# Kernel optimization log

Measured on AMD Instinct MI355X. Metric: run time of the kernel, lower is better.

## Reference

```python
import jax, jax.numpy as jnp
import numpy as np

B, C, H, W = 1, 96, 128, 128
P = 4            # patch_size
E = 192          # embed_dim
DI = 384         # d_inner = expand * embed_dim
NS = 16          # d_state
R = 12           # dt_rank = ceil(E/16)
K = 4            # scan directions
NBLK = 8         # SS2D_MBs_num
GW = C // 2      # SCPA group width


def layernorm(x, g, b, eps=1e-5):
    mu = x.mean(-1, keepdims=True)
    v = x.var(-1, keepdims=True)
    return (x - mu) * jax.lax.rsqrt(v + eps) * g + b


def batchnorm(x, g, b, m, v, eps=1e-5):
    # eval-mode BatchNorm2d over channel axis 1 of (B,C,H,W)
    return (x - m[:, None, None]) * jax.lax.rsqrt(v + eps)[:, None, None] * g[:, None, None] + b[:, None, None]


def conv2d(x, w):
    return jax.lax.conv_general_dilated(x, w, (1, 1), 'SAME', dimension_numbers=('NCHW', 'OIHW', 'NCHW'))


def dwconv2d(x, w, b):
    out = jax.lax.conv_general_dilated(x, w[:, None], (1, 1), 'SAME',
                                       dimension_numbers=('NCHW', 'OIHW', 'NCHW'),
                                       feature_group_count=w.shape[0])
    return out + b[None, :, None, None]


def lrelu(x):
    return jnp.where(x >= 0, x, 0.2 * x)


def channel_attention(x, w1, w2):
    # CBAM-style: shared MLP on avg+max pooled channel descriptors, sigmoid gate
    avg = x.mean((2, 3))
    mx = x.max((2, 3))
    mlp = lambda v: jax.nn.relu(v @ w1.T) @ w2.T
    attn = jax.nn.sigmoid(mlp(avg) + mlp(mx))
    return x * attn[:, :, None, None]


def selective_scan(xs, dts, A, Bs, Cs, Dskip):
    # xs,dts: (B,K,DI,L); A: (K,DI,NS); Bs,Cs: (B,K,NS,L); Dskip: (K,DI)
    xs_t = jnp.moveaxis(xs, -1, 0)
    dts_t = jnp.moveaxis(dts, -1, 0)
    Bs_t = jnp.moveaxis(Bs, -1, 0)
    Cs_t = jnp.moveaxis(Cs, -1, 0)
    h0 = jnp.zeros(xs.shape[:3] + (NS,), xs.dtype)  # (B,K,DI,NS)

    def step(h, t):
        xt, dt, Bt, Ct = t
        h = jnp.exp(dt[..., None] * A) * h + (dt * xt)[..., None] * Bt[:, :, None, :]
        return h, jnp.sum(h * Ct[:, :, None, :], axis=-1)

    _, ys = jax.lax.scan(step, h0, (xs_t, dts_t, Bs_t, Cs_t))
    return jnp.moveaxis(ys, 0, -1) + xs * Dskip[None, :, :, None]


def ss2d_block(x, p):
    # VMamba-style VSS block: x + SS2D(LN(x)); x: (B,Hp,Wp,E)
    (ln_g, ln_b, inproj_w, conv_w, conv_b, xproj_w, dtproj_w, dtproj_b,
     Alog, Dskip, on_g, on_b, outproj_w, merge_w) = p
    Bsz, Hp, Wp, _ = x.shape
    L = Hp * Wp
    h = layernorm(x, ln_g, ln_b)
    xz = jnp.einsum('bhwd,ed->bhwe', h, inproj_w)   # (B,Hp,Wp,2*DI)
    xc, z = jnp.split(xz, 2, axis=-1)
    xc = jax.nn.silu(dwconv2d(jnp.transpose(xc, (0, 3, 1, 2)), conv_w, conv_b))  # (B,DI,Hp,Wp)
    # 4-direction cross-scan: row-major, col-major and their reverses
    xf = xc.reshape(Bsz, DI, L)
    xwh = jnp.transpose(xc, (0, 1, 3, 2)).reshape(Bsz, DI, L)
    xs = jnp.stack([xf, xwh, jnp.flip(xf, -1), jnp.flip(xwh, -1)], axis=1)  # (B,K,DI,L)
    x_dbl = jnp.einsum('bkdl,kcd->bkcl', xs, xproj_w)  # (B,K,R+2*NS,L)
    dts, Bm, Cm = jnp.split(x_dbl, [R, R + NS], axis=2)
    dts = jax.nn.softplus(jnp.einsum('bkrl,kdr->bkdl', dts, dtproj_w) + dtproj_b[None, :, :, None])
    A = -jnp.exp(Alog)
    oy = selective_scan(xs, dts, A, Bm, Cm, Dskip)  # (B,K,DI,L)
    y0 = oy[:, 0]
    y1 = jnp.transpose(oy[:, 1].reshape(Bsz, DI, Wp, Hp), (0, 1, 3, 2)).reshape(Bsz, DI, L)
    y2 = jnp.flip(oy[:, 2], -1)
    y3 = jnp.transpose(jnp.flip(oy[:, 3], -1).reshape(Bsz, DI, Wp, Hp), (0, 1, 3, 2)).reshape(Bsz, DI, L)
    y = merge_w[0] * y0 + merge_w[1] * y1 + merge_w[2] * y2 + merge_w[3] * y3  # learnable merge
    y = jnp.transpose(y, (0, 2, 1)).reshape(Bsz, Hp, Wp, DI)
    y = layernorm(y, on_g, on_b) * jax.nn.silu(z)
    return x + jnp.einsum('bhwd,ed->bhwe', y, outproj_w)


def scpa(x, c1a, c1b, k1, k2w, k2b, k3, k4, c3):
    # PAN SCPA: two branches (3x3 conv / pixel-attention conv), 1x1 fuse, residual
    a = lrelu(jnp.einsum('bchw,oc->bohw', x, c1a))
    b = lrelu(jnp.einsum('bchw,oc->bohw', x, c1b))
    a = conv2d(a, k1)
    g = jax.nn.sigmoid(jnp.einsum('bchw,oc->bohw', b, k2w) + k2b[None, :, None, None])
    b = conv2d(conv2d(b, k3) * g, k4)
    out = jnp.einsum('bchw,oc->bohw', jnp.concatenate([lrelu(a), lrelu(b)], 1), c3)
    return out + x


def _forward(x, bn1_g, bn1_b, bn1_m, bn1_v, ca_w1, ca_w2, pe_w, pe_b, pu_w, pu_b,
             blk_ln_g, blk_ln_b, blk_inproj_w, blk_conv_w, blk_conv_b, blk_xproj_w,
             blk_dtproj_w, blk_dtproj_b, blk_Alog, blk_D, blk_on_g, blk_on_b,
             blk_outproj_w, blk_merge_w, bn2_g, bn2_b, bn2_m, bn2_v,
             scpa_c1a_w, scpa_c1b_w, scpa_k1_w, pa_k2_w, pa_k2_b, pa_k3_w, pa_k4_w, scpa_c3_w):
    residual = x
    h = batchnorm(x, bn1_g, bn1_b, bn1_m, bn1_v)
    x1 = channel_attention(h, ca_w1, ca_w2)
    Hp, Wp = H // P, W // P
    # patch embed: (B,C,H,W) -> (B,Hp,Wp,C*P*P) -> linear -> (B,Hp,Wp,E)
    xp = h.reshape(B, C, Hp, P, Wp, P).transpose(0, 2, 4, 1, 3, 5).reshape(B, Hp, Wp, C * P * P)
    x2 = xp @ pe_w.T + pe_b
    blk_params = (blk_ln_g, blk_ln_b, blk_inproj_w, blk_conv_w, blk_conv_b, blk_xproj_w,
                  blk_dtproj_w, blk_dtproj_b, blk_Alog, blk_D, blk_on_g, blk_on_b,
                  blk_outproj_w, blk_merge_w)
    x2, _ = jax.lax.scan(lambda c, p: (ss2d_block(c, p), None), x2, blk_params)
    # patch unembed
    xu = x2 @ pu_w.T + pu_b
    xu = xu.reshape(B, Hp, Wp, C, P, P).transpose(0, 3, 1, 4, 2, 5).reshape(B, C, H, W)
    xsum = residual + x1 + xu
    h2 = batchnorm(xsum, bn2_g, bn2_b, bn2_m, bn2_v)
    out = scpa(h2, scpa_c1a_w, scpa_c1b_w, scpa_k1_w, pa_k2_w, pa_k2_b, pa_k3_w, pa_k4_w, scpa_c3_w)
    return out + xsum


def setup_inputs():
    key = jax.random.key(0)
    kct = [0]
    def nk():
        kct[0] += 1
        return jax.random.fold_in(key, kct[0])
    def nrm(shape, s=0.02):
        return (jax.random.normal(nk(), shape) * s).astype(jnp.float32)
    f32 = jnp.float32
    inp = dict(
        x=jax.random.normal(nk(), (B, C, H, W), dtype=f32),
        bn1_g=jnp.ones((C,), f32), bn1_b=jnp.zeros((C,), f32),
        bn1_m=nrm((C,), 0.05), bn1_v=jnp.ones((C,), f32),
        ca_w1=nrm((C // 16, C), 0.1), ca_w2=nrm((C, C // 16), 0.1),
        pe_w=nrm((E, C * P * P)), pe_b=jnp.zeros((E,), f32),
        pu_w=nrm((C * P * P, E)), pu_b=jnp.zeros((C * P * P,), f32),
        blk_ln_g=jnp.ones((NBLK, E), f32), blk_ln_b=jnp.zeros((NBLK, E), f32),
        blk_inproj_w=nrm((NBLK, 2 * DI, E)),
        blk_conv_w=nrm((NBLK, DI, 3, 3), 0.1),
        blk_conv_b=jnp.zeros((NBLK, DI), f32),
        blk_xproj_w=nrm((NBLK, K, R + 2 * NS, DI)),
        blk_dtproj_w=nrm((NBLK, K, DI, R), 0.1),
        blk_dtproj_b=jnp.full((NBLK, K, DI), -4.6, f32),  # softplus ~= 0.01
        blk_Alog=jnp.broadcast_to(jnp.log(jnp.arange(1, NS + 1, dtype=f32)), (NBLK, K, DI, NS)) + 0.0,
        blk_D=jnp.ones((NBLK, K, DI), f32),
        blk_on_g=jnp.ones((NBLK, DI), f32), blk_on_b=jnp.zeros((NBLK, DI), f32),
        blk_outproj_w=nrm((NBLK, E, DI)),
        blk_merge_w=jnp.ones((NBLK, K), f32),
        bn2_g=jnp.ones((C,), f32), bn2_b=jnp.zeros((C,), f32),
        bn2_m=nrm((C,), 0.05), bn2_v=jnp.ones((C,), f32),
        scpa_c1a_w=nrm((GW, C), 0.05), scpa_c1b_w=nrm((GW, C), 0.05),
        scpa_k1_w=nrm((GW, GW, 3, 3), 0.05),
        pa_k2_w=nrm((GW, GW), 0.05), pa_k2_b=jnp.zeros((GW,), f32),
        pa_k3_w=nrm((GW, GW, 3, 3), 0.05), pa_k4_w=nrm((GW, GW, 3, 3), 0.05),
        scpa_c3_w=nrm((C, 2 * GW), 0.05),
    )
    return inp


def reference(x, bn1_g, bn1_b, bn1_m, bn1_v, ca_w1, ca_w2, pe_w, pe_b, pu_w, pu_b,
              blk_ln_g, blk_ln_b, blk_inproj_w, blk_conv_w, blk_conv_b, blk_xproj_w,
              blk_dtproj_w, blk_dtproj_b, blk_Alog, blk_D, blk_on_g, blk_on_b,
              blk_outproj_w, blk_merge_w, bn2_g, bn2_b, bn2_m, bn2_v,
              scpa_c1a_w, scpa_c1b_w, scpa_k1_w, pa_k2_w, pa_k2_b, pa_k3_w, pa_k4_w, scpa_c3_w):
    return _forward(x, bn1_g, bn1_b, bn1_m, bn1_v, ca_w1, ca_w2, pe_w, pe_b, pu_w, pu_b,
                    blk_ln_g, blk_ln_b, blk_inproj_w, blk_conv_w, blk_conv_b, blk_xproj_w,
                    blk_dtproj_w, blk_dtproj_b, blk_Alog, blk_D, blk_on_g, blk_on_b,
                    blk_outproj_w, blk_merge_w, bn2_g, bn2_b, bn2_m, bn2_v,
                    scpa_c1a_w, scpa_c1b_w, scpa_k1_w, pa_k2_w, pa_k2_b, pa_k3_w, pa_k4_w, scpa_c3_w)
```

## Files before the change

kernel.cpp:

```cpp
#include <hip/hip_runtime.h>
#include <math.h>

#define HW 16384
constexpr int C_ = 96;
constexpr int E_ = 192, DI_ = 384, NS_ = 16, R_ = 12, K_ = 4, NBLK_ = 8, GW_ = 48;
constexpr int L_ = 1024, CXP_ = 44;
constexpr int TC_ = 64;
constexpr int NCH_ = L_ / TC_;

__device__ __forceinline__ float lrelu_(float x){ return x >= 0.f ? x : 0.2f*x; }
__device__ __forceinline__ float sigmoid_(float x){ return 1.f/(1.f+expf(-x)); }
__device__ __forceinline__ float silu_(float x){ return x/(1.f+expf(-x)); }
__device__ __forceinline__ float softplus_(float x){ return fmaxf(x,0.f)+log1pf(expf(-fabsf(x))); }

__global__ void k_transAll(const float* __restrict__ peW, float* __restrict__ peWT,
                           const float* __restrict__ puW, float* __restrict__ puWT,
                           const float* __restrict__ inW, float* __restrict__ inWT,
                           const float* __restrict__ outW, float* __restrict__ outWT){
  __shared__ float t[32][33];
  int id = blockIdx.x;
  const float* in; float* out; int rows, cols, bx, by;
  if (id < 288){ in=peW; out=peWT; rows=192; cols=1536; bx=id%48; by=id/48; }
  else if (id < 576){ int r=id-288; in=puW; out=puWT; rows=1536; cols=192; bx=r%6; by=r/6; }
  else if (id < 1728){ int r=id-576; int z=r/144; int q=r%144;
    in=inW+(size_t)z*768*192; out=inWT+(size_t)z*768*192; rows=768; cols=192; bx=q%6; by=q/6; }
  else { int r=id-1728; int z=r/72; int q=r%72;
    in=outW+(size_t)z*192*384; out=outWT+(size_t)z*192*384; rows=192; cols=384; bx=q%12; by=q/12; }
  int r0=by*32, c0=bx*32, tx=threadIdx.x, ty=threadIdx.y;
  for (int i=0;i<32;i+=8){
    int r=r0+ty+i, c=c0+tx;
    if (r<rows && c<cols) t[ty+i][tx]=in[(size_t)r*cols+c];
  }
  __syncthreads();
  for (int i=0;i<32;i+=8){
    int c=c0+ty+i, r=r0+tx;
    if (r<rows && c<cols) out[(size_t)c*rows+r]=t[tx][ty+i];
  }
}

__global__ void k_bn1(const float* __restrict__ x, const float* g, const float* b,
                      const float* m, const float* v,
                      float* __restrict__ h, float* __restrict__ stats,
                      float* __restrict__ su, float* __restrict__ sq){
  int c = blockIdx.x, tid = threadIdx.x;
  int gid = c*256 + tid;
  if (gid < 1024){ su[gid] = 0.f; sq[gid] = 0.f; }
  float sc = g[c]*rsqrtf(v[c]+1e-5f), sh = b[c]-m[c]*sc;
  const float* xc = x + (size_t)c*HW;
  float* hc = h + (size_t)c*HW;
  float s = 0.f, mx = -1e30f;
  for (int i=tid;i<HW;i+=256){
    float val = fmaf(xc[i], sc, sh);
    hc[i] = val; s += val; mx = fmaxf(mx, val);
  }
  for (int o=32;o;o>>=1){ s += __shfl_xor(s,o); mx = fmaxf(mx, __shfl_xor(mx,o)); }
  __shared__ float ss[4], sm[4];
  int wid = tid>>6, lane = tid&63;
  if (!lane){ ss[wid]=s; sm[wid]=mx; }
  __syncthreads();
  if (!tid){
    stats[c] = (ss[0]+ss[1]+ss[2]+ss[3])*(1.f/HW);
    stats[96+c] = fmaxf(fmaxf(sm[0],sm[1]),fmaxf(sm[2],sm[3]));
  }
}

__global__ void k_attn(const float* __restrict__ stats, const float* __restrict__ w1,
                       const float* __restrict__ w2, float* __restrict__ attn){
  __shared__ float hid[12];
  int tid = threadIdx.x;
  if (tid < 12){
    int j = tid%6, which = tid/6;
    const float* vv = stats + which*96;
    float a = 0.f;
    for (int c=0;c<96;c++) a += vv[c]*w1[j*96+c];
    hid[tid] = fmaxf(a, 0.f);
  }
  __syncthreads();
  if (tid < 96){
    float a = 0.f;
    for (int j=0;j<6;j++) a += (hid[j]+hid[6+j])*w2[tid*6+j];
    attn[tid] = sigmoid_(a);
  }
}

__global__ __launch_bounds__(256) void k_gemmPE(const float* __restrict__ hsrc,
                      const float* __restrict__ wt, const float* __restrict__ bias,
                      float* __restrict__ out, float* __restrict__ su, float* __restrict__ sq){
  const int K = 1536, N = 192;
  __shared__ float As[32][34];
  __shared__ float Bs[32][32];
  int tid = threadIdx.x;
  int m0 = blockIdx.x*32, n0 = blockIdx.y*32;
  int tx = tid&15, ty = tid>>4;
  int arow = tid>>3, akq = tid&7;
  int brow = tid>>3, bn4 = tid&7;
  int m = m0+arow;
  int base2 = (m>>5)*512 + (m&31)*4;
  auto aload = [&](int kk)->float4 {
    int c = kk>>4, i2 = (kk>>2)&3;
    return *(const float4*)&hsrc[((size_t)c<<14) + (size_t)(i2*128 + base2)];
  };
  float4 aR = aload(akq*4);
  float4 bR = *(const float4*)&wt[(size_t)brow*N + n0 + bn4*4];
  float acc[2][2] = {{0}};
  for (int k0=0; k0<K; k0+=32){
    __syncthreads();
    As[akq*4+0][arow]=aR.x; As[akq*4+1][arow]=aR.y;
    As[akq*4+2][arow]=aR.z; As[akq*4+3][arow]=aR.w;
    *(float4*)&Bs[brow][bn4*4] = bR;
    __syncthreads();
    if (k0+32 < K){
      aR = aload(k0+32+akq*4);
      bR = *(const float4*)&wt[(size_t)(k0+32+brow)*N + n0 + bn4*4];
    }
    #pragma unroll
    for (int kk=0; kk<32; kk++){
      float2 av = *(const float2*)&As[kk][ty*2];
      float2 bv = *(const float2*)&Bs[kk][tx*2];
      acc[0][0] = fmaf(av.x, bv.x, acc[0][0]);
      acc[0][1] = fmaf(av.x, bv.y, acc[0][1]);
      acc[1][0] = fmaf(av.y, bv.x, acc[1][0]);
      acc[1][1] = fmaf(av.y, bv.y, acc[1][1]);
    }
  }
  float2 bq = *(const float2*)&bias[n0+tx*2];
  float sl[2], ql[2];
  #pragma unroll
  for (int i=0;i<2;i++){
    size_t o = (size_t)(m0+ty*2+i)*N + n0 + tx*2;
    float2 ov; ov.x = acc[i][0]+bq.x; ov.y = acc[i][1]+bq.y;
    *(float2*)&out[o] = ov;
    sl[i] = ov.x+ov.y; ql[i] = ov.x*ov.x+ov.y*ov.y;
  }
  #pragma unroll
  for (int o=8;o;o>>=1){
    sl[0]+=__shfl_xor(sl[0],o); ql[0]+=__shfl_xor(ql[0],o);
    sl[1]+=__shfl_xor(sl[1],o); ql[1]+=__shfl_xor(ql[1],o);
  }
  if (tx==0){
    atomicAdd(&su[m0+ty*2],   sl[0]); atomicAdd(&sq[m0+ty*2],   ql[0]);
    atomicAdd(&su[m0+ty*2+1], sl[1]); atomicAdd(&sq[m0+ty*2+1], ql[1]);
  }
}

__global__ __launch_bounds__(256) void k_gemm32s(const float* __restrict__ act,
                      const float* __restrict__ wt, const float* __restrict__ res,
                      float* __restrict__ out, float* __restrict__ su, float* __restrict__ sq,
                      int K, int N){
  __shared__ float As[32][34];
  __shared__ float Bs[32][32];
  int tid = threadIdx.x;
  int m0 = blockIdx.x*32, n0 = blockIdx.y*32;
  int tx = tid&15, ty = tid>>4;
  int arow = tid>>3, akq = tid&7;
  int brow = tid>>3, bn4 = tid&7;
  float4 aR = *(const float4*)&act[(size_t)(m0+arow)*K + akq*4];
  float4 bR = *(const float4*)&wt [(size_t)brow*N + n0 + bn4*4];
  float acc[2][2] = {{0}};
  for (int k0=0; k0<K; k0+=32){
    __syncthreads();
    As[akq*4+0][arow]=aR.x; As[akq*4+1][arow]=aR.y;
    As[akq*4+2][arow]=aR.z; As[akq*4+3][arow]=aR.w;
    *(float4*)&Bs[brow][bn4*4] = bR;
    __syncthreads();
    if (k0+32 < K){
      aR = *(const float4*)&act[(size_t)(m0+arow)*K + k0+32 + akq*4];
      bR = *(const float4*)&wt [(size_t)(k0+32+brow)*N + n0 + bn4*4];
    }
    #pragma unroll
    for (int kk=0; kk<32; kk++){
      float2 av = *(const float2*)&As[kk][ty*2];
      float2 bv = *(const float2*)&Bs[kk][tx*2];
      acc[0][0] = fmaf(av.x, bv.x, acc[0][0]);
      acc[0][1] = fmaf(av.x, bv.y, acc[0][1]);
      acc[1][0] = fmaf(av.y, bv.x, acc[1][0]);
      acc[1][1] = fmaf(av.y, bv.y, acc[1][1]);
    }
  }
  float sl[2], ql[2];
  #pragma unroll
  for (int i=0;i<2;i++){
    size_t o = (size_t)(m0+ty*2+i)*N + n0 + tx*2;
    float2 r = *(const float2*)&res[o];
    float2 ov; ov.x = acc[i][0]+r.x; ov.y = acc[i][1]+r.y;
    *(float2*)&out[o] = ov;
    sl[i] = ov.x+ov.y; ql[i] = ov.x*ov.x+ov.y*ov.y;
  }
  #pragma unroll
  for (int o=8;o;o>>=1){
    sl[0]+=__shfl_xor(sl[0],o); ql[0]+=__shfl_xor(ql[0],o);
    sl[1]+=__shfl_xor(sl[1],o); ql[1]+=__shfl_xor(ql[1],o);
  }
  if (tx==0){
    atomicAdd(&su[m0+ty*2],   sl[0]); atomicAdd(&sq[m0+ty*2],   ql[0]);
    atomicAdd(&su[m0+ty*2+1], sl[1]); atomicAdd(&sq[m0+ty*2+1], ql[1]);
  }
}

__global__ __launch_bounds__(256) void k_gemmPU(const float* __restrict__ act,
                      const float* __restrict__ wt, const float* __restrict__ bias,
                      float* __restrict__ out){
  const int K = 192, N = 1536;
  __shared__ float As[32][34];
  __shared__ float Bs[32][32];
  int tid = threadIdx.x;
  int m0 = blockIdx.x*32, n0 = blockIdx.y*32;
  int tx = tid&15, ty = tid>>4;
  int arow = tid>>3, akq = tid&7;
  int brow = tid>>3, bn4 = tid&7;
  float4 aR = *(const float4*)&act[(size_t)(m0+arow)*K + akq*4];
  float4 bR = *(const float4*)&wt [(size_t)brow*N + n0 + bn4*4];
  float acc[2][2] = {{0}};
  for (int k0=0; k0<K; k0+=32){
    __syncthreads();
    As[akq*4+0][arow]=aR.x; As[akq*4+1][arow]=aR.y;
    As[akq*4+2][arow]=aR.z; As[akq*4+3][arow]=aR.w;
    *(float4*)&Bs[brow][bn4*4] = bR;
    __syncthreads();
    if (k0+32 < K){
      aR = *(const float4*)&act[(size_t)(m0+arow)*K + k0+32 + akq*4];
      bR = *(const float4*)&wt [(size_t)(k0+32+brow)*N + n0 + bn4*4];
    }
    #pragma unroll
    for (int kk=0; kk<32; kk++){
      float2 av = *(const float2*)&As[kk][ty*2];
      float2 bv = *(const float2*)&Bs[kk][tx*2];
      acc[0][0] = fmaf(av.x, bv.x, acc[0][0]);
      acc[0][1] = fmaf(av.x, bv.y, acc[0][1]);
      acc[1][0] = fmaf(av.y, bv.x, acc[1][0]);
      acc[1][1] = fmaf(av.y, bv.y, acc[1][1]);
    }
  }
  int n = n0 + tx*2;
  float2 bq = *(const float2*)&bias[n];
  int c = n>>4, i2 = (n>>2)&3, j = n&3;
  #pragma unroll
  for (int i=0;i<2;i++){
    int m = m0+ty*2+i;
    size_t o = ((size_t)c<<14) + (size_t)((m>>5)*4+i2)*128 + (m&31)*4 + j;
    float2 ov; ov.x = acc[i][0]+bq.x; ov.y = acc[i][1]+bq.y;
    *(float2*)&out[o] = ov;
  }
}

__global__ __launch_bounds__(256) void k_gemm32ln(const float* __restrict__ act,
                      const float* __restrict__ wt, const float* __restrict__ lg,
                      const float* __restrict__ lb, const float* __restrict__ su,
                      const float* __restrict__ sq, float* __restrict__ out,
                      int K, int N){
  __shared__ float As[32][34];
  __shared__ float Bs[32][32];
  int tid = threadIdx.x;
  int m0 = blockIdx.x*32, n0 = blockIdx.y*32;
  int tx = tid&15, ty = tid>>4;
  int arow = tid>>3, akq = tid&7;
  int brow = tid>>3, bn4 = tid&7;
  float m = su[m0+arow]*(1.f/192.f);
  float r = rsqrtf(sq[m0+arow]*(1.f/192.f) - m*m + 1e-5f);
  float4 aR = *(const float4*)&act[(size_t)(m0+arow)*K + akq*4];
  float4 gR = *(const float4*)&lg[akq*4];
  float4 hR = *(const float4*)&lb[akq*4];
  float4 bR = *(const float4*)&wt[(size_t)brow*N + n0 + bn4*4];
  float acc[2][2] = {{0}};
  for (int k0=0; k0<K; k0+=32){
    __syncthreads();
    As[akq*4+0][arow] = (aR.x-m)*r*gR.x + hR.x;
    As[akq*4+1][arow] = (aR.y-m)*r*gR.y + hR.y;
    As[akq*4+2][arow] = (aR.z-m)*r*gR.z + hR.z;
    As[akq*4+3][arow] = (aR.w-m)*r*gR.w + hR.w;
    *(float4*)&Bs[brow][bn4*4] = bR;
    __syncthreads();
    if (k0+32 < K){
      aR = *(const float4*)&act[(size_t)(m0+arow)*K + k0+32 + akq*4];
      gR = *(const float4*)&lg[k0+32+akq*4];
      hR = *(const float4*)&lb[k0+32+akq*4];
      bR = *(const float4*)&wt[(size_t)(k0+32+brow)*N + n0 + bn4*4];
    }
    #pragma unroll
    for (int kk=0; kk<32; kk++){
      float2 av = *(const float2*)&As[kk][ty*2];
      float2 bv = *(const float2*)&Bs[kk][tx*2];
      acc[0][0] = fmaf(av.x, bv.x, acc[0][0]);
      acc[0][1] = fmaf(av.x, bv.y, acc[0][1]);
      acc[1][0] = fmaf(av.y, bv.x, acc[1][0]);
      acc[1][1] = fmaf(av.y, bv.y, acc[1][1]);
    }
  }
  #pragma unroll
  for (int i=0;i<2;i++){
    size_t o = (size_t)(m0+ty*2+i)*N + n0 + tx*2;
    float2 ov; ov.x = acc[i][0]; ov.y = acc[i][1];
    *(float2*)&out[o] = ov;
  }
}

__global__ __launch_bounds__(256) void k_dwxst(const float* __restrict__ xz,
                        const float* __restrict__ w, const float* __restrict__ bias,
                        float* __restrict__ xcs, float* __restrict__ xst0,
                        float* __restrict__ xst1){
  __shared__ float ld[96][33];
  __shared__ float t[32][33];
  int h0 = blockIdx.x;
  int d0 = blockIdx.y*32;
  int tx = threadIdx.x, ty = threadIdx.y;
  #pragma unroll
  for (int i=0;i<12;i++){
    int ll = i*8 + ty;
    int h = h0 - 1 + (ll>>5);
    int wv = ll & 31;
    float v = 0.f;
    if ((unsigned)h < 32u) v = xz[(size_t)(h*32+wv)*768 + d0 + tx];
    ld[ll][tx] = v;
  }
  __syncthreads();
  #pragma unroll
  for (int i=0;i<4;i++){
    int dl = ty + 8*i;
    int d = d0 + dl;
    float acc = bias[d];
    const float* wp = w + d*9;
    #pragma unroll
    for (int di=0;di<3;di++){
      #pragma unroll
      for (int dj=0;dj<3;dj++){
        int wq = tx + dj - 1;
        if ((unsigned)wq < 32u)
          acc = fmaf(ld[di*32 + wq][dl], wp[di*3+dj], acc);
      }
    }
    float val = silu_(acc);
    xcs[(size_t)d*L_ + h0*32 + tx] = val;
    t[dl][tx] = val;
  }
  __syncthreads();
  int d = d0 + tx;
  #pragma unroll
  for (int i=0;i<4;i++){
    int wq = ty + 8*i;
    int l = h0*32 + wq;
    float val = t[tx][wq];
    int t1 = wq*32 + h0;
    xst0[(size_t)l*DI_ + d] = val;
    xst1[(size_t)t1*DI_ + d] = val;
  }
}

__global__ __launch_bounds__(256) void k_xdblP(const float* __restrict__ xcs,
                       const float* __restrict__ xw, float* __restrict__ xdblP){
  int kz = blockIdx.z;
  int k = kz & 3, sp = kz >> 2;
  int s = blockIdx.x*256 + threadIdx.x;
  int Ts = ((s&31)<<5) | (s>>5);
  int lw;
  if (k==0) lw = s;
  else if (k==1) lw = Ts;
  else if (k==2) lw = 1023-s;
  else lw = 1023-Ts;
  int c0 = blockIdx.y*4;
  const float* wp = xw + ((size_t)k*CXP_ + c0)*DI_ + sp*128;
  const float* src = xcs + s + (size_t)sp*128*L_;
  float a0=0,a1=0,a2=0,a3=0;
  for (int d=0; d<128; d++){
    float v = src[(size_t)d*L_];
    a0 = fmaf(v, wp[d],        a0);
    a1 = fmaf(v, wp[DI_+d],    a1);
    a2 = fmaf(v, wp[2*DI_+d],  a2);
    a3 = fmaf(v, wp[3*DI_+d],  a3);
  }
  size_t base = (((size_t)sp*4 + k)*CXP_ + c0)*L_ + lw;
  xdblP[base]       = a0;
  xdblP[base+L_]    = a1;
  xdblP[base+2*L_]  = a2;
  xdblP[base+3*L_]  = a3;
}

__global__ void k_dtbc(const float* __restrict__ xdblP, const float* __restrict__ dtw,
                       const float* __restrict__ dtb, float* __restrict__ dts_t,
                       float* __restrict__ bc){
  int k = blockIdx.y, l = blockIdx.x, d = threadIdx.x;
  const float* p0 = xdblP + ((size_t)(0+k)*CXP_)*L_ + l;
  const float* p1 = xdblP + ((size_t)(4+k)*CXP_)*L_ + l;
  const float* p2 = xdblP + ((size_t)(8+k)*CXP_)*L_ + l;
  float acc = dtb[(size_t)k*DI_ + d];
  const float* w = dtw + ((size_t)k*DI_ + d)*R_;
  #pragma unroll
  for (int r=0;r<R_;r++){
    size_t o = (size_t)r*L_;
    acc = fmaf(p0[o]+p1[o]+p2[o], w[r], acc);
  }
  dts_t[((size_t)k*L_ + l)*DI_ + d] = softplus_(acc);
  if (d < 32){
    size_t o = (size_t)(R_+d)*L_;
    bc[((size_t)k*L_ + l)*32 + d] = p0[o]+p1[o]+p2[o];
  }
}

__global__ __launch_bounds__(256) void k_scanA(const float* __restrict__ xst0,
                      const float* __restrict__ xst1,
                      const float* __restrict__ dts_t, const float* __restrict__ bc,
                      const float* __restrict__ Alog,
                      float* __restrict__ Ech, float* __restrict__ Hch){
  int k = blockIdx.z;
  int d = blockIdx.y*16 + (threadIdx.x>>4);
  int n = threadIdx.x&15;
  int ch = blockIdx.x;
  float A = -expf(Alog[((size_t)k*DI_ + d)*NS_ + n]);
  float aL2 = A * 1.4426950408889634f;
  int t0 = ch*TC_;
  const float* dtp = dts_t + ((size_t)k*L_ + t0)*DI_ + d;
  const float* bcp = bc    + ((size_t)k*L_ + t0)*32;
  const float* xb = (k&1) ? xst1 : xst0;
  const float* xp_; ptrdiff_t xs_;
  if (k < 2){ xp_ = xb + (size_t)t0*DI_ + d; xs_ = DI_; }
  else      { xp_ = xb + (size_t)(1023-t0)*DI_ + d; xs_ = -(ptrdiff_t)DI_; }
  float h = 0.f, Ep = 1.f;
  #pragma unroll 4
  for (int t=0;t<TC_;t++){
    float dt = dtp[(size_t)t*DI_];
    float xv = xp_[(ptrdiff_t)t*xs_];
    float Bn = bcp[t*32+n];
    float e = exp2f(aL2*dt);
    h = fmaf(e, h, dt*xv*Bn);
    Ep *= e;
  }
  size_t idx = (((size_t)k*NCH_ + ch)*DI_ + d)*NS_ + n;
  Ech[idx] = Ep; Hch[idx] = h;
}

__global__ __launch_bounds__(256) void k_scanC(const float* __restrict__ xst0,
                      const float* __restrict__ xst1,
                      const float* __restrict__ dts_t, const float* __restrict__ bc,
                      const float* __restrict__ Alog,
                      const float* __restrict__ Ech, const float* __restrict__ Hch,
                      float* __restrict__ yst){
  int k = blockIdx.z;
  int d = blockIdx.y*16 + (threadIdx.x>>4);
  int n = threadIdx.x&15;
  int ch = blockIdx.x;
  float A = -expf(Alog[((size_t)k*DI_ + d)*NS_ + n]);
  float aL2 = A * 1.4426950408889634f;
  int t0 = ch*TC_;
  const float* dtp = dts_t + ((size_t)k*L_ + t0)*DI_ + d;
  const float* bcp = bc    + ((size_t)k*L_ + t0)*32;
  const float* xb = (k&1) ? xst1 : xst0;
  const float* xp_; ptrdiff_t xs_;
  if (k < 2){ xp_ = xb + (size_t)t0*DI_ + d; xs_ = DI_; }
  else      { xp_ = xb + (size_t)(1023-t0)*DI_ + d; xs_ = -(ptrdiff_t)DI_; }
  float* yp = yst + ((size_t)k*L_ + t0)*DI_ + d;
  float h = 0.f;
  size_t dn = ((size_t)k*NCH_*DI_ + d)*0;
  for (int c=0;c<ch;c++){
    size_t o = (((size_t)k*NCH_ + c)*DI_ + d)*NS_ + n;
    h = fmaf(Ech[o], h, Hch[o]);
  }
  (void)dn;
  #pragma unroll 4
  for (int t=0;t<TC_;t++){
    float dt = dtp[(size_t)t*DI_];
    float xv = xp_[(ptrdiff_t)t*xs_];
    float Bn = bcp[t*32+n], Cn = bcp[t*32+16+n];
    float e = exp2f(aL2*dt);
    h = fmaf(e, h, dt*xv*Bn);
    float p = h*Cn;
    p += __shfl_xor(p,1); p += __shfl_xor(p,2);
    p += __shfl_xor(p,4); p += __shfl_xor(p,8);
    if (n==0) yp[(size_t)t*DI_] = p;
  }
}

__global__ void k_merge(const float* __restrict__ yst, const float* __restrict__ xst0,
                        const float* __restrict__ xst1,
                        const float* __restrict__ Dsk, const float* __restrict__ mw,
                        const float* __restrict__ ong, const float* __restrict__ onb,
                        const float* __restrict__ xz, float* __restrict__ out,
                        float* __restrict__ su, float* __restrict__ sq){
  int l = blockIdx.x, d = threadIdx.x;
  if (d == 0){ su[l] = 0.f; sq[l] = 0.f; }
  int T = ((l&31)<<5) | (l>>5);
  int tt[4] = { l, T, 1023-l, 1023-T };
  float xv0 = xst0[(size_t)l*DI_ + d];
  float xv1 = xst1[(size_t)T*DI_ + d];
  float v = 0.f;
  #pragma unroll
  for (int k=0;k<4;k++){
    float xk = (k&1) ? xv1 : xv0;
    v += mw[k]*(yst[(size_t)(k*L_ + tt[k])*DI_ + d] + xk*Dsk[k*DI_+d]);
  }
  float s = v, sqv = v*v;
  for (int o=32;o;o>>=1){ s += __shfl_xor(s,o); sqv += __shfl_xor(sqv,o); }
  __shared__ float rs_[6], rq_[6];
  int lane = d&63, wid = d>>6;
  if (!lane){ rs_[wid]=s; rq_[wid]=sqv; }
  __syncthreads();
  float ts=0.f, tq=0.f;
  #pragma unroll
  for (int i=0;i<6;i++){ ts += rs_[i]; tq += rq_[i]; }
  float mu = ts*(1.f/DI_);
  float rstd = rsqrtf(tq*(1.f/DI_) - mu*mu + 1e-5f);
  float y = (v-mu)*rstd*ong[d] + onb[d];
  float z = xz[(size_t)l*768 + DI_ + d];
  out[(size_t)l*DI_ + d] = y * silu_(z);
}

__global__ void k_sum(const float* __restrict__ x, const float* __restrict__ h,
                      const float* __restrict__ attn, const float* __restrict__ xu,
                      const float* g2, const float* b2, const float* m2, const float* v2,
                      float* __restrict__ xsum, float* __restrict__ h2){
  int idx = blockIdx.x*256 + threadIdx.x;
  int c = idx>>14;
  float s = x[idx] + h[idx]*attn[c] + xu[idx];
  xsum[idx] = s;
  h2[idx] = (s - m2[c])*rsqrtf(v2[c]+1e-5f)*g2[c] + b2[c];
}

__global__ __launch_bounds__(256) void k_1x1ab(const float* __restrict__ h2,
                        const float* __restrict__ wa, const float* __restrict__ wb,
                        float* __restrict__ a, float* __restrict__ b){
  __shared__ float lw[96*12];
  int ocg = blockIdx.y;
  for (int i=threadIdx.x; i<96*12; i+=256){
    int o = i%12, c = i/12;
    lw[i] = (o<6) ? wa[(ocg*6 + o)*96 + c] : wb[(ocg*6 + (o-6))*96 + c];
  }
  __syncthreads();
  int p = blockIdx.x*256 + threadIdx.x;
  float acc[12];
  #pragma unroll
  for (int o=0;o<12;o++) acc[o]=0.f;
  for (int c=0;c<96;c++){
    float v = h2[(size_t)c*HW + p];
    const float* w = lw + c*12;
    #pragma unroll
    for (int o=0;o<12;o++) acc[o] = fmaf(v, w[o], acc[o]);
  }
  #pragma unroll
  for (int o=0;o<6;o++){
    a[(size_t)(ocg*6+o)*HW + p] = lrelu_(acc[o]);
    b[(size_t)(ocg*6+o)*HW + p] = lrelu_(acc[6+o]);
  }
}

__global__ __launch_bounds__(256) void k_1x1g(const float* __restrict__ b,
                       const float* __restrict__ w, const float* __restrict__ bias,
                       float* __restrict__ g){
  __shared__ float lw[48*6];
  int ocg = blockIdx.y;
  for (int i=threadIdx.x; i<48*6; i+=256){
    int o = i%6, c = i/6;
    lw[i] = w[(ocg*6 + o)*48 + c];
  }
  __syncthreads();
  int p = blockIdx.x*256 + threadIdx.x;
  float acc[6];
  #pragma unroll
  for (int o=0;o<6;o++) acc[o] = bias[ocg*6+o];
  for (int c=0;c<48;c++){
    float v = b[(size_t)c*HW + p];
    const float* wp = lw + c*6;
    #pragma unroll
    for (int o=0;o<6;o++) acc[o] = fmaf(v, wp[o], acc[o]);
  }
  #pragma unroll
  for (int o=0;o<6;o++) g[(size_t)(ocg*6+o)*HW + p] = sigmoid_(acc[o]);
}

__global__ __launch_bounds__(256) void k_conv3d(const float* __restrict__ inA,
                        const float* __restrict__ wA, const float* __restrict__ inB,
                        const float* __restrict__ wB, const float* __restrict__ aux,
                        float* __restrict__ outA, float* __restrict__ outB){
  __shared__ float lw[48*9*6];
  __shared__ float ld[8][4][130];
  int sp = blockIdx.x;
  int half = blockIdx.y >> 3;
  int ocg = blockIdx.y & 7;
  const float* in = half ? inB : inA;
  const float* w  = half ? wB : wA;
  int tid = threadIdx.x;
  for (int i=tid; i<48*9*6; i+=256){
    int o = i%6, j = (i/6)%9, ic = i/54;
    lw[i] = w[((size_t)(ocg*6+o)*48 + ic)*9 + j];
  }
  if (tid < 32){ ld[tid>>2][tid&3][0] = 0.f; ld[tid>>2][tid&3][129] = 0.f; }
  int p = sp*256 + tid;
  int ww = p&127;
  int hbase = sp*2 - 1;
  int lr = 1 + (tid>>7);
  float acc[6];
  #pragma unroll
  for (int o=0;o<6;o++) acc[o]=0.f;
  for (int ic0=0; ic0<48; ic0+=8){
    __syncthreads();
    #pragma unroll
    for (int q=0;q<16;q++){
      int i = tid + q*256;
      int icl = i>>9, rem = i&511;
      int r = rem>>7, cp = rem&127;
      int gy = hbase + r;
      ld[icl][r][cp+1] = ((unsigned)gy < 128u) ? in[(size_t)(ic0+icl)*HW + gy*128 + cp] : 0.f;
    }
    __syncthreads();
    #pragma unroll
    for (int icl=0; icl<8; icl++){
      const float* lwp = lw + (ic0+icl)*54;
      #pragma unroll
      for (int di=0;di<3;di++){
        #pragma unroll
        for (int dj=0;dj<3;dj++){
          float xv = ld[icl][lr-1+di][ww+dj];
          const float* wj = lwp + (di*3+dj)*6;
          #pragma unroll
          for (int o=0;o<6;o++) acc[o] = fmaf(xv, wj[o], acc[o]);
        }
      }
    }
  }
  if (half == 0){
    #pragma unroll
    for (int o=0;o<6;o++)
      outA[(size_t)(ocg*6+o)*HW + p] = lrelu_(acc[o]);
  } else {
    #pragma unroll
    for (int o=0;o<6;o++){
      size_t oi = (size_t)(ocg*6+o)*HW + p;
      outB[oi] = acc[o]*aux[oi];
    }
  }
}

__global__ __launch_bounds__(256) void k_conv3(const float* __restrict__ in,
                        const float* __restrict__ w, float* __restrict__ out){
  __shared__ float lw[48*9*6];
  __shared__ float ld[8][4][130];
  int sp = blockIdx.x;
  int ocg = blockIdx.y;
  int tid = threadIdx.x;
  for (int i=tid; i<48*9*6; i+=256){
    int o = i%6, j = (i/6)%9, ic = i/54;
    lw[i] = w[((size_t)(ocg*6+o)*48 + ic)*9 + j];
  }
  if (tid < 32){ ld[tid>>2][tid&3][0] = 0.f; ld[tid>>2][tid&3][129] = 0.f; }
  int p = sp*256 + tid;
  int ww = p&127;
  int hbase = sp*2 - 1;
  int lr = 1 + (tid>>7);
  float acc[6];
  #pragma unroll
  for (int o=0;o<6;o++) acc[o]=0.f;
  for (int ic0=0; ic0<48; ic0+=8){
    __syncthreads();
    #pragma unroll
    for (int q=0;q<16;q++){
      int i = tid + q*256;
      int icl = i>>9, rem = i&511;
      int r = rem>>7, cp = rem&127;
      int gy = hbase + r;
      ld[icl][r][cp+1] = ((unsigned)gy < 128u) ? in[(size_t)(ic0+icl)*HW + gy*128 + cp] : 0.f;
    }
    __syncthreads();
    #pragma unroll
    for (int icl=0; icl<8; icl++){
      const float* lwp = lw + (ic0+icl)*54;
      #pragma unroll
      for (int di=0;di<3;di++){
        #pragma unroll
        for (int dj=0;dj<3;dj++){
          float xv = ld[icl][lr-1+di][ww+dj];
          const float* wj = lwp + (di*3+dj)*6;
          #pragma unroll
          for (int o=0;o<6;o++) acc[o] = fmaf(xv, wj[o], acc[o]);
        }
      }
    }
  }
  #pragma unroll
  for (int o=0;o<6;o++)
    out[(size_t)(ocg*6+o)*HW + p] = lrelu_(acc[o]);
}

__global__ __launch_bounds__(256) void k_c3(const float* __restrict__ ab,
                     const float* __restrict__ w, const float* __restrict__ h2,
                     const float* __restrict__ xsum, float* __restrict__ out){
  __shared__ float lw[96*12];
  int ocg = blockIdx.y;
  for (int i=threadIdx.x; i<96*12; i+=256){
    int o = i%12, j = i/12;
    lw[i] = w[(ocg*12 + o)*96 + j];
  }
  __syncthreads();
  int p = blockIdx.x*256 + threadIdx.x;
  float acc[12];
  #pragma unroll
  for (int o=0;o<12;o++) acc[o]=0.f;
  for (int j=0;j<96;j++){
    float v = ab[(size_t)j*HW + p];
    const float* wp = lw + j*12;
    #pragma unroll
    for (int o=0;o<12;o++) acc[o] = fmaf(v, wp[o], acc[o]);
  }
  #pragma unroll
  for (int o=0;o<12;o++){
    size_t oi = (size_t)(ocg*12+o)*HW + p;
    out[oi] = acc[o] + h2[oi] + xsum[oi];
  }
}

extern "C" void kernel_launch(void* const* d_in, const int* in_sizes, int n_in,
                              void* d_out, int out_size, void* d_ws, size_t ws_size,
                              hipStream_t stream){
  (void)in_sizes; (void)n_in; (void)out_size; (void)ws_size;
  const float* x    = (const float*)d_in[0];
  const float* bn1g = (const float*)d_in[1];
  const float* bn1b = (const float*)d_in[2];
  const float* bn1m = (const float*)d_in[3];
  const float* bn1v = (const float*)d_in[4];
  const float* caw1 = (const float*)d_in[5];
  const float* caw2 = (const float*)d_in[6];
  const float* peW  = (const float*)d_in[7];
  const float* peb  = (const float*)d_in[8];
  const float* puW  = (const float*)d_in[9];
  const float* pub  = (const float*)d_in[10];
  const float* lng  = (const float*)d_in[11];
  const float* lnb  = (const float*)d_in[12];
  const float* inW  = (const float*)d_in[13];
  const float* convw= (const float*)d_in[14];
  const float* convb= (const float*)d_in[15];
  const float* xprojw=(const float*)d_in[16];
  const float* dtw  = (const float*)d_in[17];
  const float* dtb  = (const float*)d_in[18];
  const float* Alog = (const float*)d_in[19];
  const float* Dsk  = (const float*)d_in[20];
  const float* ong  = (const float*)d_in[21];
  const float* onb  = (const float*)d_in[22];
  const float* outW = (const float*)d_in[23];
  const float* mw   = (const float*)d_in[24];
  const float* bn2g = (const float*)d_in[25];
  const float* bn2b = (const float*)d_in[26];
  const float* bn2m = (const float*)d_in[27];
  const float* bn2v = (const float*)d_in[28];
  const float* c1a  = (const float*)d_in[29];
  const float* c1b  = (const float*)d_in[30];
  const float* k1w  = (const float*)d_in[31];
  const float* k2w  = (const float*)d_in[32];
  const float* k2b  = (const float*)d_in[33];
  const float* k3w  = (const float*)d_in[34];
  const float* k4w  = (const float*)d_in[35];
  const float* c3w  = (const float*)d_in[36];
  float* out = (float*)d_out;

  float* ws = (float*)d_ws;
  size_t off = 0;
  auto alloc = [&](size_t n){ float* p = ws + off; off += n; return p; };
  float* peWT  = alloc((size_t)1536*192);
  float* puWT  = alloc((size_t)192*1536);
  float* inWT  = alloc((size_t)8*192*768);
  float* outWT = alloc((size_t)8*384*192);
  float* bufH  = alloc((size_t)96*HW);
  float* stats = alloc(256);
  float* attn  = alloc(128);
  float* bufP  = alloc((size_t)1024*1536);
  float* x2a   = alloc((size_t)1024*192);
  float* x2b   = alloc((size_t)1024*192);
  float* bufXZ = alloc((size_t)1024*768);
  float* bufXCS= alloc((size_t)384*1024);
  float* bufXST= alloc((size_t)4*1024*384);
  float* xdblP = alloc((size_t)12*44*1024);
  float* dts   = alloc((size_t)4*1024*384);
  float* bc    = alloc((size_t)4*1024*32);
  float* yst   = alloc((size_t)4*1024*384);
  float* bufY  = alloc((size_t)1024*384);
  float* xsum  = alloc((size_t)96*HW);
  float* h2    = alloc((size_t)96*HW);
  float* Ech   = alloc((size_t)K_*NCH_*DI_*NS_);
  float* Hch   = alloc((size_t)K_*NCH_*DI_*NS_);
  float* suB   = alloc(1024);
  float* sqB   = alloc(1024);
  float* xst0  = bufXST;
  float* xst1  = bufXST + (size_t)L_*DI_;

  dim3 tb(32,8);
  k_transAll<<<2304, tb, 0, stream>>>(peW, peWT, puW, puWT, inW, inWT, outW, outWT);

  k_bn1<<<96,256,0,stream>>>(x, bn1g, bn1b, bn1m, bn1v, bufH, stats, suB, sqB);
  k_attn<<<1,128,0,stream>>>(stats, caw1, caw2, attn);
  k_gemmPE<<<dim3(32,6),256,0,stream>>>(bufH, peWT, peb, x2a, suB, sqB);

  float* cur = x2a; float* nxt = x2b;
  for (int b=0;b<8;b++){
    k_gemm32ln<<<dim3(32,24),256,0,stream>>>(cur, inWT+(size_t)b*192*768,
                        lng+(size_t)b*192, lnb+(size_t)b*192, suB, sqB, bufXZ, 192, 768);
    k_dwxst<<<dim3(32,12),tb,0,stream>>>(bufXZ, convw+(size_t)b*384*9,
                        convb+(size_t)b*384, bufXCS, xst0, xst1);
    k_xdblP<<<dim3(4,11,12),256,0,stream>>>(bufXCS, xprojw+(size_t)b*4*44*384, xdblP);
    k_dtbc<<<dim3(1024,4),384,0,stream>>>(xdblP, dtw+(size_t)b*4*384*12, dtb+(size_t)b*4*384, dts, bc);
    const float* Ab = Alog + (size_t)b*4*384*16;
    k_scanA<<<dim3(NCH_,DI_/16,4),256,0,stream>>>(xst0, xst1, dts, bc, Ab, Ech, Hch);
    k_scanC<<<dim3(NCH_,DI_/16,4),256,0,stream>>>(xst0, xst1, dts, bc, Ab, Ech, Hch, yst);
    k_merge<<<1024,384,0,stream>>>(yst, xst0, xst1, Dsk+(size_t)b*4*384, mw+(size_t)b*4,
                                   ong+(size_t)b*384, onb+(size_t)b*384, bufXZ, bufY, suB, sqB);
    k_gemm32s<<<dim3(32,6),256,0,stream>>>(bufY, outWT+(size_t)b*384*192, cur, nxt, suB, sqB, 384, 192);
    float* t = cur; cur = nxt; nxt = t;
  }

  k_gemmPU<<<dim3(32,48),256,0,stream>>>(cur, puWT, pub, bufP);
  k_sum<<<(96*HW)/256,256,0,stream>>>(x, bufH, attn, bufP, bn2g, bn2b, bn2m, bn2v, xsum, h2);

  float* bufA = dts;
  float* bufB = dts + (size_t)48*HW;
  float* bufG = yst;
  float* bufT = yst + (size_t)48*HW;
  float* ab   = bufXST;
  k_1x1ab<<<dim3(64,8),256,0,stream>>>(h2, c1a, c1b, bufA, bufB);
  k_1x1g<<<dim3(64,8),256,0,stream>>>(bufB, k2w, k2b, bufG);
  k_conv3d<<<dim3(64,16),256,0,stream>>>(bufA, k1w, bufB, k3w, bufG, ab, bufT);
  k_conv3<<<dim3(64,8),256,0,stream>>>(bufT, k4w, ab+(size_t)48*HW);
  k_c3<<<dim3(64,8),256,0,stream>>>(ab, c3w, h2, xsum, out);
}
```

Measured before the change: 1.204 ms.

## Add carry-propagation scan pass and fuse sigmoid gate 1x1 into conv3d

```diff
diff --git a/kernel.cpp b/kernel.cpp
--- a/kernel.cpp
+++ b/kernel.cpp
@@ -427,11 +427,24 @@
   Ech[idx] = Ep; Hch[idx] = h;
 }
 
+__global__ void k_scanB(const float* __restrict__ Ech, const float* __restrict__ Hch,
+                        float* __restrict__ carry){
+  int idx = blockIdx.x*256 + threadIdx.x;
+  int k = idx / (DI_*NS_);
+  int dn = idx % (DI_*NS_);
+  float h = 0.f;
+  #pragma unroll
+  for (int c=0;c<NCH_;c++){
+    size_t o = ((size_t)(k*NCH_+c)*DI_*NS_) + dn;
+    carry[o] = h;
+    h = fmaf(Ech[o], h, Hch[o]);
+  }
+}
+
 __global__ __launch_bounds__(256) void k_scanC(const float* __restrict__ xst0,
                       const float* __restrict__ xst1,
                       const float* __restrict__ dts_t, const float* __restrict__ bc,
-                      const float* __restrict__ Alog,
-                      const float* __restrict__ Ech, const float* __restrict__ Hch,
+                      const float* __restrict__ Alog, const float* __restrict__ carry,
                       float* __restrict__ yst){
   int k = blockIdx.z;
   int d = blockIdx.y*16 + (threadIdx.x>>4);
@@ -447,13 +460,7 @@
   if (k < 2){ xp_ = xb + (size_t)t0*DI_ + d; xs_ = DI_; }
   else      { xp_ = xb + (size_t)(1023-t0)*DI_ + d; xs_ = -(ptrdiff_t)DI_; }
   float* yp = yst + ((size_t)k*L_ + t0)*DI_ + d;
-  float h = 0.f;
-  size_t dn = ((size_t)k*NCH_*DI_ + d)*0;
-  for (int c=0;c<ch;c++){
-    size_t o = (((size_t)k*NCH_ + c)*DI_ + d)*NS_ + n;
-    h = fmaf(Ech[o], h, Hch[o]);
-  }
-  (void)dn;
+  float h = carry[(((size_t)k*NCH_ + ch)*DI_ + d)*NS_ + n];
   #pragma unroll 4
   for (int t=0;t<TC_;t++){
     float dt = dtp[(size_t)t*DI_];
@@ -540,35 +547,13 @@
   }
 }
 
-__global__ __launch_bounds__(256) void k_1x1g(const float* __restrict__ b,
-                       const float* __restrict__ w, const float* __restrict__ bias,
-                       float* __restrict__ g){
-  __shared__ float lw[48*6];
-  int ocg = blockIdx.y;
-  for (int i=threadIdx.x; i<48*6; i+=256){
-    int o = i%6, c = i/6;
-    lw[i] = w[(ocg*6 + o)*48 + c];
-  }
-  __syncthreads();
-  int p = blockIdx.x*256 + threadIdx.x;
-  float acc[6];
-  #pragma unroll
-  for (int o=0;o<6;o++) acc[o] = bias[ocg*6+o];
-  for (int c=0;c<48;c++){
-    float v = b[(size_t)c*HW + p];
-    const float* wp = lw + c*6;
-    #pragma unroll
-    for (int o=0;o<6;o++) acc[o] = fmaf(v, wp[o], acc[o]);
-  }
-  #pragma unroll
-  for (int o=0;o<6;o++) g[(size_t)(ocg*6+o)*HW + p] = sigmoid_(acc[o]);
-}
-
 __global__ __launch_bounds__(256) void k_conv3d(const float* __restrict__ inA,
                         const float* __restrict__ wA, const float* __restrict__ inB,
-                        const float* __restrict__ wB, const float* __restrict__ aux,
+                        const float* __restrict__ wB,
+                        const float* __restrict__ k2w, const float* __restrict__ k2b,
                         float* __restrict__ outA, float* __restrict__ outB){
   __shared__ float lw[48*9*6];
+  __shared__ float lg[48*6];
   __shared__ float ld[8][4][130];
   int sp = blockIdx.x;
   int half = blockIdx.y >> 3;
@@ -580,14 +565,20 @@
     int o = i%6, j = (i/6)%9, ic = i/54;
     lw[i] = w[((size_t)(ocg*6+o)*48 + ic)*9 + j];
   }
+  if (half){
+    for (int i=tid; i<48*6; i+=256){
+      int o = i%6, c = i/6;
+      lg[i] = k2w[(ocg*6 + o)*48 + c];
+    }
+  }
   if (tid < 32){ ld[tid>>2][tid&3][0] = 0.f; ld[tid>>2][tid&3][129] = 0.f; }
   int p = sp*256 + tid;
   int ww = p&127;
   int hbase = sp*2 - 1;
   int lr = 1 + (tid>>7);
-  float acc[6];
-  #pragma unroll
-  for (int o=0;o<6;o++) acc[o]=0.f;
+  float acc[6], gacc[6];
+  #pragma unroll
+  for (int o=0;o<6;o++){ acc[o]=0.f; gacc[o]=0.f; }
   for (int ic0=0; ic0<48; ic0+=8){
     __syncthreads();
     #pragma unroll
@@ -612,6 +603,12 @@
           for (int o=0;o<6;o++) acc[o] = fmaf(xv, wj[o], acc[o]);
         }
       }
+      if (half){
+        float cv = ld[icl][lr][ww+1];
+        const float* gj = lg + (ic0+icl)*6;
+        #pragma unroll
+        for (int o=0;o<6;o++) gacc[o] = fmaf(cv, gj[o], gacc[o]);
+      }
     }
   }
   if (half == 0){
@@ -622,7 +619,7 @@
     #pragma unroll
     for (int o=0;o<6;o++){
       size_t oi = (size_t)(ocg*6+o)*HW + p;
-      outB[oi] = acc[o]*aux[oi];
+      outB[oi] = acc[o]*sigmoid_(gacc[o] + k2b[ocg*6+o]);
     }
   }
 }
@@ -772,6 +769,7 @@
   float* h2    = alloc((size_t)96*HW);
   float* Ech   = alloc((size_t)K_*NCH_*DI_*NS_);
   float* Hch   = alloc((size_t)K_*NCH_*DI_*NS_);
+  float* carry = alloc((size_t)K_*NCH_*DI_*NS_);
   float* suB   = alloc(1024);
   float* sqB   = alloc(1024);
   float* xst0  = bufXST;
@@ -794,7 +792,8 @@
     k_dtbc<<<dim3(1024,4),384,0,stream>>>(xdblP, dtw+(size_t)b*4*384*12, dtb+(size_t)b*4*384, dts, bc);
     const float* Ab = Alog + (size_t)b*4*384*16;
     k_scanA<<<dim3(NCH_,DI_/16,4),256,0,stream>>>(xst0, xst1, dts, bc, Ab, Ech, Hch);
-    k_scanC<<<dim3(NCH_,DI_/16,4),256,0,stream>>>(xst0, xst1, dts, bc, Ab, Ech, Hch, yst);
+    k_scanB<<<(K_*DI_*NS_)/256,256,0,stream>>>(Ech, Hch, carry);
+    k_scanC<<<dim3(NCH_,DI_/16,4),256,0,stream>>>(xst0, xst1, dts, bc, Ab, carry, yst);
     k_merge<<<1024,384,0,stream>>>(yst, xst0, xst1, Dsk+(size_t)b*4*384, mw+(size_t)b*4,
                                    ong+(size_t)b*384, onb+(size_t)b*384, bufXZ, bufY, suB, sqB);
     k_gemm32s<<<dim3(32,6),256,0,stream>>>(bufY, outWT+(size_t)b*384*192, cur, nxt, suB, sqB, 384, 192);
@@ -806,12 +805,10 @@
 
   float* bufA = dts;
   float* bufB = dts + (size_t)48*HW;
-  float* bufG = yst;
-  float* bufT = yst + (size_t)48*HW;
+  float* bufT = yst;
   float* ab   = bufXST;
   k_1x1ab<<<dim3(64,8),256,0,stream>>>(h2, c1a, c1b, bufA, bufB);
-  k_1x1g<<<dim3(64,8),256,0,stream>>>(bufB, k2w, k2b, bufG);
-  k_conv3d<<<dim3(64,16),256,0,stream>>>(bufA, k1w, bufB, k3w, bufG, ab, bufT);
+  k_conv3d<<<dim3(64,16),256,0,stream>>>(bufA, k1w, bufB, k3w, k2w, k2b, ab, bufT);
   k_conv3<<<dim3(64,8),256,0,stream>>>(bufT, k4w, ab+(size_t)48*HW);
   k_c3<<<dim3(64,8),256,0,stream>>>(ab, c3w, h2, xsum, out);
 }
```

Measured after the change: 1.273 ms. 1.06x slower.
